# Kernel tuning notes

Hardware: AMD Instinct MI355X
Metric: run time of the kernel (lower is better)

## Reference

```python
import jax, jax.numpy as jnp
import numpy as np

LAMBDA_SOFTMAX = 10.0  # opt.lambda_softmax
LEAKY_SLOPE = 0.1


def l2norm(x, axis):
    # matches torch F.normalize(p=2, eps=1e-12)
    n = jnp.linalg.norm(x, axis=axis, keepdims=True)
    return x / jnp.clip(n, 1e-12)


def setup_inputs() -> dict:
    key = jax.random.key(0)
    k1, k2, k3, k4, k5 = jax.random.split(key, 5)
    I, Q, T, S, D = 64, 49, 64, 64, 256  # n_img, n_region, n_txt, max_words, feature_size
    return {
        "local_img_query": jax.random.normal(k1, (I, Q, D), jnp.float32),
        "local_img_value": jax.random.normal(k2, (I, Q, D), jnp.float32),
        "local_text_key": jax.random.normal(k3, (T, S, D), jnp.float32),
        "local_text_value": jax.random.normal(k4, (T, S, D), jnp.float32),
        "text_length": jax.random.randint(k5, (T,), 8, S + 1, jnp.int32),
    }


def reference(local_img_query, local_img_value, local_text_key, local_text_value, text_length):
    # Vectorized form of the per-sentence Python loop in compute_i2t_sim.
    # Variable sentence lengths are handled with a mask over the padded word axis,
    # which reproduces the ragged torch math exactly (see comments).
    T, S, D = local_text_key.shape
    I, Q, _ = local_img_query.shape

    qn = l2norm(local_img_query, -1)   # [I,Q,D]
    kn = l2norm(local_text_key, -1)    # [T,S,D]

    # bmm(txt_key_norm, queryT): (B,S,D)x(B,D,Q) -> here [T,I,S,Q]
    attn = jnp.einsum('tsd,iqd->tisq', kn, qn)
    attn = jnp.where(attn > 0, attn, LEAKY_SLOPE * attn)      # LeakyReLU(0.1)
    # l2norm(attn, 2) normalizes over queryL per (t,i,s) row -> independent of padding
    attn = l2norm(attn, -1)
    attn = jnp.swapaxes(attn, 2, 3)                            # [T,I,Q,S]

    mask = jnp.arange(S)[None, :] < text_length[:, None]       # [T,S]
    logits = jnp.where(mask[:, None, None, :], attn * LAMBDA_SOFTMAX, -jnp.inf)
    attn = jax.nn.softmax(logits, axis=-1)                     # padded words -> exactly 0

    # focal_equal with sourceL = actual n_word of each sentence
    n_word = text_length.astype(attn.dtype)[:, None, None, None]
    funcF = attn * n_word - jnp.sum(attn, axis=-1, keepdims=True)
    fattn = (funcF > 0).astype(attn.dtype)                     # padded attn=0 -> funcF<0 -> 0
    tmp = fattn * attn
    attn = tmp / jnp.sum(tmp, axis=-1, keepdims=True)

    # bmm(valueT, attnT) -> weighted text context per (txt, img): [T,I,Q,D]
    wei = jnp.einsum('tsd,tiqs->tiqd', local_text_value, attn)
    wei = l2norm(wei, -1)

    # cosine similarity with image values along d, then mean over regions
    v = local_img_value[None]                                  # [1,I,Q,D]
    w12 = jnp.sum(v * wei, -1)
    denom = jnp.linalg.norm(v, axis=-1) * jnp.linalg.norm(wei, axis=-1)
    sim = w12 / jnp.clip(denom, 1e-8)                          # [T,I,Q]
    i2t = sim.mean(axis=-1)                                    # [T,I]
    return i2t.T                                               # [n_img, n_txt]
```

## Files before the change

### kernel.cpp

```cpp
#include <hip/hip_runtime.h>
#include <math.h>

#define I_N 64
#define Q_N 49
#define T_N 64
#define S_N 64
#define D_N 256

typedef __attribute__((ext_vector_type(8))) short short8;
typedef __attribute__((ext_vector_type(4))) float f32x4;
typedef unsigned short ushort_t;

__device__ __forceinline__ float waveReduceSum64(float v) {
    v += __shfl_xor(v, 1);
    v += __shfl_xor(v, 2);
    v += __shfl_xor(v, 4);
    v += __shfl_xor(v, 8);
    v += __shfl_xor(v, 16);
    v += __shfl_xor(v, 32);
    return v;
}

__device__ __forceinline__ ushort_t f2bf(float x) {
    unsigned u = __builtin_bit_cast(unsigned, x);
    unsigned r = (u + 0x7fffu + ((u >> 16) & 1u)) >> 16;
    return (ushort_t)r;
}
__device__ __forceinline__ float bf2f(ushort_t h) {
    unsigned u = ((unsigned)h) << 16;
    return __builtin_bit_cast(float, u);
}
__device__ __forceinline__ void split_bf16(float x, ushort_t& h, ushort_t& l) {
    h = f2bf(x);
    l = f2bf(x - bf2f(h));
}

__global__ void prep_norm(const float* __restrict__ q_in, const float* __restrict__ v_in,
                          const float* __restrict__ k_in,
                          ushort_t* __restrict__ qfh, ushort_t* __restrict__ qfl,
                          ushort_t* __restrict__ kfh, ushort_t* __restrict__ kfl,
                          float* __restrict__ vnorm) {
    int b = blockIdx.x;
    int tid = threadIdx.x;
    int isimg = (b < 4096) ? 1 : 0;
    int row = isimg ? b : (b - 4096);
    int hi = row >> 6, lo = row & 63;
    float x = 0.0f, vv = 0.0f;
    if (isimg) {
        if (lo < Q_N) {
            size_t base = ((size_t)hi * Q_N + lo) * D_N + tid;
            x = q_in[base];
            vv = v_in[base];
        }
    } else {
        x = k_in[(size_t)row * D_N + tid];
    }
    __shared__ float ws[8];
    float s1 = waveReduceSum64(x * x);
    float s2 = waveReduceSum64(vv * vv);
    int wv = tid >> 6, ln = tid & 63;
    if (ln == 0) { ws[wv] = s1; ws[4 + wv] = s2; }
    __syncthreads();
    float n1 = sqrtf(ws[0] + ws[1] + ws[2] + ws[3]);
    float xn = x / fmaxf(n1, 1e-12f);
    ushort_t h, l;
    split_bf16(xn, h, l);
    size_t off = ((size_t)hi << 14) + (size_t)((((lo >> 4) * 8 + (tid >> 5))) << 9)
               + (size_t)(((((tid >> 3) & 3) * 16 + (lo & 15))) << 3) + (tid & 7);
    if (isimg) {
        qfh[off] = h;
        qfl[off] = l;
        if (tid == 0) vnorm[row] = sqrtf(ws[4] + ws[5] + ws[6] + ws[7]);
    } else {
        kfh[off] = h;
        kfl[off] = l;
    }
}

__global__ void prep_vt(const float* __restrict__ tv,
                        ushort_t* __restrict__ vfh, ushort_t* __restrict__ vfl) {
    __shared__ float tile[64][65];
    int t = blockIdx.x;
    int d0 = blockIdx.y * 64;
    int tid = threadIdx.x;
    const float* src = tv + ((size_t)t << 14) + d0;
    ushort_t* dh = vfh + ((size_t)t << 14);
    ushort_t* dl = vfl + ((size_t)t << 14);
#pragma unroll
    for (int r = 0; r < 16; ++r) {
        int idx = r * 256 + tid;
        int s = idx >> 6, d = idx & 63;
        tile[s][d] = src[s * D_N + d];
    }
    __syncthreads();
#pragma unroll
    for (int r = 0; r < 16; ++r) {
        int idx = r * 256 + tid;
        int d = idx >> 6, s = idx & 63;
        int dg = d0 + d;
        float x = tile[s][d];
        ushort_t h, l;
        split_bf16(x, h, l);
        int w = dg >> 5, md = (dg >> 4) & 1, lrd = dg & 15;
        int k0g = s >> 5, lk = (s >> 3) & 3, e = s & 7;
        size_t off = (size_t)(w << 11) + (k0g << 10) + (md << 9) + lk * 128 + lrd * 8 + e;
        dh[off] = h;
        dl[off] = l;
    }
}

__global__ void prep_vp(const float* __restrict__ vimg, float* __restrict__ vP) {
    int i = blockIdx.x;
    int tid = threadIdx.x;
    const float* src = vimg + (size_t)i * Q_N * D_N;
    float* dst = vP + ((size_t)i << 14);
#pragma unroll
    for (int rep = 0; rep < 2; ++rep) {
        int p = rep * 256 + tid;
        int w = p >> 6, lane = p & 63;
        int lr = lane & 15, lk = lane >> 4;
        float* d0 = dst + (size_t)p * 32;
#pragma unroll
        for (int nq = 0; nq < 4; ++nq) {
            int q = nq * 16 + lr;
#pragma unroll
            for (int md = 0; md < 2; ++md)
#pragma unroll
                for (int r = 0; r < 4; ++r) {
                    int d = w * 32 + md * 16 + lk * 4 + r;
                    d0[nq * 8 + md * 4 + r] = (q < Q_N) ? src[q * D_N + d] : 0.0f;
                }
        }
    }
}

__launch_bounds__(512, 6)
__global__ void i2t_mfma(const ushort_t* __restrict__ kfh, const ushort_t* __restrict__ kfl,
                         const ushort_t* __restrict__ qfh, const ushort_t* __restrict__ qfl,
                         const ushort_t* __restrict__ vfh, const ushort_t* __restrict__ vfl,
                         const float* __restrict__ vP,
                         const float* __restrict__ vnorm,
                         const int* __restrict__ tlen,
                         float* __restrict__ out)
{
    __shared__ __align__(16) unsigned char RK[33280];

    const int bid = blockIdx.x;
    const int xcd = bid & 7;
    const int j = bid >> 3;
    const int t = (xcd << 3) | (j & 7);
    const int i = j >> 3;

    const int tid = threadIdx.x;
    const int lane = tid & 63;
    const int w = tid >> 6;
    const int lr = lane & 15;
    const int lk = lane >> 4;

    const int wsr = (w >> 2) * 32;
    const int wq  = (w & 3) * 16;
    f32x4 acc[2];
    acc[0] = (f32x4){0.f, 0.f, 0.f, 0.f};
    acc[1] = (f32x4){0.f, 0.f, 0.f, 0.f};
    {
        const ushort_t* kH = kfh + ((size_t)t << 14) + (size_t)(w >> 2) * 8192;
        const ushort_t* kL = kfl + ((size_t)t << 14) + (size_t)(w >> 2) * 8192;
        const ushort_t* qH = qfh + ((size_t)i << 14) + (size_t)(w & 3) * 4096;
        const ushort_t* qL = qfl + ((size_t)i << 14) + (size_t)(w & 3) * 4096;
#pragma unroll
        for (int k8 = 0; k8 < 8; ++k8) {
            int fo = k8 * 512 + lane * 8;
            short8 aH0 = *(const short8*)(kH + fo);
            short8 aL0 = *(const short8*)(kL + fo);
            short8 aH1 = *(const short8*)(kH + 4096 + fo);
            short8 aL1 = *(const short8*)(kL + 4096 + fo);
            short8 bH  = *(const short8*)(qH + fo);
            short8 bL  = *(const short8*)(qL + fo);
            acc[0] = __builtin_amdgcn_mfma_f32_16x16x32_bf16(aH0, bH, acc[0], 0, 0, 0);
            acc[0] = __builtin_amdgcn_mfma_f32_16x16x32_bf16(aH0, bL, acc[0], 0, 0, 0);
            acc[0] = __builtin_amdgcn_mfma_f32_16x16x32_bf16(aL0, bH, acc[0], 0, 0, 0);
            acc[1] = __builtin_amdgcn_mfma_f32_16x16x32_bf16(aH1, bH, acc[1], 0, 0, 0);
            acc[1] = __builtin_amdgcn_mfma_f32_16x16x32_bf16(aH1, bL, acc[1], 0, 0, 0);
            acc[1] = __builtin_amdgcn_mfma_f32_16x16x32_bf16(aL1, bH, acc[1], 0, 0, 0);
        }
    }
    {
        float* As = (float*)RK;
#pragma unroll
        for (int mi = 0; mi < 2; ++mi)
#pragma unroll
            for (int r = 0; r < 4; ++r) {
                int s = wsr + mi * 16 + lk * 4 + r;
                int q = wq + lr;
                float v = acc[mi][r];
                v = (v > 0.0f) ? v : 0.1f * v;
                As[s * 65 + q] = v;
            }
    }
    __syncthreads();

    {
        const float* As = (const float*)RK;
        float* rinv = (float*)(RK + 16640);
        int s = tid >> 3, part = tid & 7;
        float ss = 0.0f;
#pragma unroll
        for (int q0 = 0; q0 < 64; q0 += 8) {
            float v = As[s * 65 + q0 + part];
            ss += v * v;
        }
        ss += __shfl_xor(ss, 1);
        ss += __shfl_xor(ss, 2);
        ss += __shfl_xor(ss, 4);
        if (part == 0) rinv[s] = 1.0f / fmaxf(sqrtf(ss), 1e-12f);
    }
    __syncthreads();

    const int len = tlen[t];
    {
        const float* As = (const float*)RK;
        const float* rinv = (const float*)(RK + 16640);
        ushort_t* Ph = (ushort_t*)(RK + 16896);
        ushort_t* Pl = (ushort_t*)(RK + 25088);
        const float thr = 1.0f / (float)len;
        int q = tid >> 3, part = tid & 7;
        float logit[8];
        float m = -INFINITY;
#pragma unroll
        for (int k = 0; k < 8; ++k) {
            int s = part * 8 + k;
            float lg = (s < len) ? 10.0f * As[s * 65 + q] * rinv[s] : -INFINITY;
            logit[k] = lg;
            m = fmaxf(m, lg);
        }
        m = fmaxf(m, __shfl_xor(m, 1));
        m = fmaxf(m, __shfl_xor(m, 2));
        m = fmaxf(m, __shfl_xor(m, 4));
        float p[8];
        float sum = 0.0f;
#pragma unroll
        for (int k = 0; k < 8; ++k) {
            int s = part * 8 + k;
            float e = (s < len) ? __expf(logit[k] - m) : 0.0f;
            p[k] = e;
            sum += e;
        }
        sum += __shfl_xor(sum, 1);
        sum += __shfl_xor(sum, 2);
        sum += __shfl_xor(sum, 4);
        float inv = 1.0f / sum;
        float sk = 0.0f;
#pragma unroll
        for (int k = 0; k < 8; ++k) {
            p[k] *= inv;
            if (p[k] > thr) sk += p[k];
        }
        sk += __shfl_xor(sk, 1);
        sk += __shfl_xor(sk, 2);
        sk += __shfl_xor(sk, 4);
        float iv2 = 1.0f / sk;

        short8 vh, vl;
#pragma unroll
        for (int k = 0; k < 8; ++k) {
            float pv = (p[k] > thr) ? p[k] * iv2 : 0.0f;
            if (q >= Q_N) pv = 0.0f;
            ushort_t hh, ll;
            split_bf16(pv, hh, ll);
            vh[k] = (short)hh;
            vl[k] = (short)ll;
        }
        int o = q * 64 + ((part ^ (q & 7)) << 3);
        *(short8*)(Ph + o) = vh;
        *(short8*)(Pl + o) = vl;
    }
    __syncthreads();

    f32x4 acc2[4][2];
#pragma unroll
    for (int a = 0; a < 4; ++a)
#pragma unroll
        for (int b = 0; b < 2; ++b) acc2[a][b] = (f32x4){0.f, 0.f, 0.f, 0.f};
    {
        const ushort_t* vH = vfh + ((size_t)t << 14) + (size_t)w * 2048;
        const ushort_t* vL = vfl + ((size_t)t << 14) + (size_t)w * 2048;
        const ushort_t* PH = (const ushort_t*)(RK + 16896);
        const ushort_t* PL = (const ushort_t*)(RK + 25088);
#pragma unroll
        for (int k0g = 0; k0g < 2; ++k0g) {
#pragma unroll
            for (int md = 0; md < 2; ++md) {
                int vo = k0g * 1024 + md * 512 + lane * 8;
                short8 vh = *(const short8*)(vH + vo);
                short8 vl = *(const short8*)(vL + vo);
#pragma unroll
                for (int nq = 0; nq < 4; ++nq) {
                    int q = nq * 16 + lr;
                    int o = q * 64 + (((k0g * 4 + lk) ^ (q & 7)) << 3);
                    short8 ph = *(const short8*)(PH + o);
                    short8 pl = *(const short8*)(PL + o);
                    acc2[nq][md] = __builtin_amdgcn_mfma_f32_16x16x32_bf16(vh, ph, acc2[nq][md], 0, 0, 0);
                    acc2[nq][md] = __builtin_amdgcn_mfma_f32_16x16x32_bf16(vl, ph, acc2[nq][md], 0, 0, 0);
                    acc2[nq][md] = __builtin_amdgcn_mfma_f32_16x16x32_bf16(vh, pl, acc2[nq][md], 0, 0, 0);
                }
            }
        }
    }

    {
        float* wsq = (float*)RK;
        float* wdv = (float*)(RK + 2048);
        const float* vPb = vP + ((((size_t)i * 8 + w) * 64 + lane) << 5);
#pragma unroll
        for (int nq = 0; nq < 4; ++nq) {
            f32x4 v0 = *(const f32x4*)(vPb + nq * 8);
            f32x4 v1 = *(const f32x4*)(vPb + nq * 8 + 4);
            float s2 = 0.0f, dv = 0.0f;
#pragma unroll
            for (int r = 0; r < 4; ++r) {
                float w0 = acc2[nq][0][r];
                float w1 = acc2[nq][1][r];
                s2 += w0 * w0 + w1 * w1;
                dv += w0 * v0[r] + w1 * v1[r];
            }
            s2 += __shfl_xor(s2, 16);
            s2 += __shfl_xor(s2, 32);
            dv += __shfl_xor(dv, 16);
            dv += __shfl_xor(dv, 32);
            if (lane < 16) {
                wsq[w * 64 + nq * 16 + lane] = s2;
                wdv[w * 64 + nq * 16 + lane] = dv;
            }
        }
    }
    __syncthreads();
    if (tid < 64) {
        const float* wsq = (const float*)RK;
        const float* wdv = (const float*)(RK + 2048);
        int q = tid;
        float s2 = 0.0f, dv = 0.0f;
#pragma unroll
        for (int ww = 0; ww < 8; ++ww) {
            s2 += wsq[ww * 64 + q];
            dv += wdv[ww * 64 + q];
        }
        float sim = 0.0f;
        if (q < Q_N) {
            float wn = sqrtf(s2);
            float w12 = dv / fmaxf(wn, 1e-12f);
            float wnn = wn / fmaxf(wn, 1e-12f);
            float denom = fmaxf(vnorm[i * 64 + q] * wnn, 1e-8f);
            sim = w12 / denom;
        }
        sim = waveReduceSum64(sim);
        if (tid == 0) out[(size_t)i * T_N + t] = sim * (1.0f / (float)Q_N);
    }
}

extern "C" void kernel_launch(void* const* d_in, const int* in_sizes, int n_in,
                              void* d_out, int out_size, void* d_ws, size_t ws_size,
                              hipStream_t stream) {
    const float* img_query = (const float*)d_in[0];
    const float* img_value = (const float*)d_in[1];
    const float* text_key  = (const float*)d_in[2];
    const float* text_val  = (const float*)d_in[3];
    const int*   text_len  = (const int*)d_in[4];
    float* out = (float*)d_out;

    const size_t NPAD = (size_t)64 * 64 * 256;
    ushort_t* qfh = (ushort_t*)d_ws;
    ushort_t* qfl = qfh + NPAD;
    ushort_t* kfh = qfl + NPAD;
    ushort_t* kfl = kfh + NPAD;
    ushort_t* vfh = kfl + NPAD;
    ushort_t* vfl = vfh + NPAD;
    float* vnorm  = (float*)(vfl + NPAD);
    float* vP     = vnorm + I_N * 64;

    prep_norm<<<8192, 256, 0, stream>>>(img_query, img_value, text_key,
                                        qfh, qfl, kfh, kfl, vnorm);
    prep_vt<<<dim3(T_N, 4), 256, 0, stream>>>(text_val, vfh, vfl);
    prep_vp<<<I_N, 256, 0, stream>>>(img_value, vP);

    i2t_mfma<<<T_N * I_N, 512, 0, stream>>>(kfh, kfl, qfh, qfl, vfh, vfl,
                                            vP, vnorm, text_len, out);
}
```

Before: 129.1 us.

## Halve block size to 4 waves with larger per-wave MFMA tiles and fragment reuse

The main kernel now runs 256 threads (4 waves) per block instead of 512. Each wave computes a 32x32 output tile in the first GEMM and covers 64 feature columns in the second, so loaded A/B fragments and softmax P fragments are reused across more MFMAs. The prep kernels change the V-text and V-image packed layouts to match the new per-wave ownership, and the softmax stage uses 4 threads per row instead of 8. In exchange each wave holds more registers (acc2 grows to 16 f32x4) and occupancy per CU may drop.

```diff
diff --git a/kernel.cpp b/kernel.cpp
--- a/kernel.cpp
+++ b/kernel.cpp
@@ -101,9 +101,9 @@
         float x = tile[s][d];
         ushort_t h, l;
         split_bf16(x, h, l);
-        int w = dg >> 5, md = (dg >> 4) & 1, lrd = dg & 15;
-        int k0g = s >> 5, lk = (s >> 3) & 3, e = s & 7;
-        size_t off = (size_t)(w << 11) + (k0g << 10) + (md << 9) + lk * 128 + lrd * 8 + e;
+        int dgrp = dg >> 4, lrd = dg & 15;
+        int k0g = s >> 5, lk3 = (s >> 3) & 3, e = s & 7;
+        size_t off = (size_t)(dgrp << 10) + (k0g << 9) + ((lk3 * 16 + lrd) << 3) + e;
         dh[off] = h;
         dl[off] = l;
     }
@@ -113,28 +113,23 @@
     int i = blockIdx.x;
     int tid = threadIdx.x;
     const float* src = vimg + (size_t)i * Q_N * D_N;
-    float* dst = vP + ((size_t)i << 14);
-#pragma unroll
-    for (int rep = 0; rep < 2; ++rep) {
-        int p = rep * 256 + tid;
-        int w = p >> 6, lane = p & 63;
-        int lr = lane & 15, lk = lane >> 4;
-        float* d0 = dst + (size_t)p * 32;
-#pragma unroll
-        for (int nq = 0; nq < 4; ++nq) {
-            int q = nq * 16 + lr;
-#pragma unroll
-            for (int md = 0; md < 2; ++md)
-#pragma unroll
-                for (int r = 0; r < 4; ++r) {
-                    int d = w * 32 + md * 16 + lk * 4 + r;
-                    d0[nq * 8 + md * 4 + r] = (q < Q_N) ? src[q * D_N + d] : 0.0f;
-                }
-        }
-    }
-}
-
-__launch_bounds__(512, 6)
+    int wv = tid >> 6, lane = tid & 63;
+    int lr = lane & 15, lk = lane >> 4;
+    float* d0 = vP + ((size_t)i << 14) + (size_t)tid * 64;
+#pragma unroll
+    for (int nq = 0; nq < 4; ++nq) {
+        int q = nq * 16 + lr;
+#pragma unroll
+        for (int md = 0; md < 4; ++md)
+#pragma unroll
+            for (int r = 0; r < 4; ++r) {
+                int d = wv * 64 + md * 16 + lk * 4 + r;
+                d0[nq * 16 + md * 4 + r] = (q < Q_N) ? src[q * D_N + d] : 0.0f;
+            }
+    }
+}
+
+__launch_bounds__(256, 4)
 __global__ void i2t_mfma(const ushort_t* __restrict__ kfh, const ushort_t* __restrict__ kfl,
                          const ushort_t* __restrict__ qfh, const ushort_t* __restrict__ qfl,
                          const ushort_t* __restrict__ vfh, const ushort_t* __restrict__ vfl,
@@ -157,16 +152,18 @@
     const int lr = lane & 15;
     const int lk = lane >> 4;
 
-    const int wsr = (w >> 2) * 32;
-    const int wq  = (w & 3) * 16;
-    f32x4 acc[2];
-    acc[0] = (f32x4){0.f, 0.f, 0.f, 0.f};
-    acc[1] = (f32x4){0.f, 0.f, 0.f, 0.f};
-    {
-        const ushort_t* kH = kfh + ((size_t)t << 14) + (size_t)(w >> 2) * 8192;
-        const ushort_t* kL = kfl + ((size_t)t << 14) + (size_t)(w >> 2) * 8192;
-        const ushort_t* qH = qfh + ((size_t)i << 14) + (size_t)(w & 3) * 4096;
-        const ushort_t* qL = qfl + ((size_t)i << 14) + (size_t)(w & 3) * 4096;
+    const int wsr = (w >> 1) * 32;
+    const int wq  = (w & 1) * 32;
+    f32x4 acc[2][2];
+#pragma unroll
+    for (int a = 0; a < 2; ++a)
+#pragma unroll
+        for (int b = 0; b < 2; ++b) acc[a][b] = (f32x4){0.f, 0.f, 0.f, 0.f};
+    {
+        const ushort_t* kH = kfh + ((size_t)t << 14) + (size_t)(w >> 1) * 8192;
+        const ushort_t* kL = kfl + ((size_t)t << 14) + (size_t)(w >> 1) * 8192;
+        const ushort_t* qH = qfh + ((size_t)i << 14) + (size_t)(w & 1) * 8192;
+        const ushort_t* qL = qfl + ((size_t)i << 14) + (size_t)(w & 1) * 8192;
 #pragma unroll
         for (int k8 = 0; k8 < 8; ++k8) {
             int fo = k8 * 512 + lane * 8;
@@ -174,44 +171,53 @@
             short8 aL0 = *(const short8*)(kL + fo);
             short8 aH1 = *(const short8*)(kH + 4096 + fo);
             short8 aL1 = *(const short8*)(kL + 4096 + fo);
-            short8 bH  = *(const short8*)(qH + fo);
-            short8 bL  = *(const short8*)(qL + fo);
-            acc[0] = __builtin_amdgcn_mfma_f32_16x16x32_bf16(aH0, bH, acc[0], 0, 0, 0);
-            acc[0] = __builtin_amdgcn_mfma_f32_16x16x32_bf16(aH0, bL, acc[0], 0, 0, 0);
-            acc[0] = __builtin_amdgcn_mfma_f32_16x16x32_bf16(aL0, bH, acc[0], 0, 0, 0);
-            acc[1] = __builtin_amdgcn_mfma_f32_16x16x32_bf16(aH1, bH, acc[1], 0, 0, 0);
-            acc[1] = __builtin_amdgcn_mfma_f32_16x16x32_bf16(aH1, bL, acc[1], 0, 0, 0);
-            acc[1] = __builtin_amdgcn_mfma_f32_16x16x32_bf16(aL1, bH, acc[1], 0, 0, 0);
+            short8 bH0 = *(const short8*)(qH + fo);
+            short8 bL0 = *(const short8*)(qL + fo);
+            short8 bH1 = *(const short8*)(qH + 4096 + fo);
+            short8 bL1 = *(const short8*)(qL + 4096 + fo);
+            acc[0][0] = __builtin_amdgcn_mfma_f32_16x16x32_bf16(aH0, bH0, acc[0][0], 0, 0, 0);
+            acc[0][1] = __builtin_amdgcn_mfma_f32_16x16x32_bf16(aH0, bH1, acc[0][1], 0, 0, 0);
+            acc[1][0] = __builtin_amdgcn_mfma_f32_16x16x32_bf16(aH1, bH0, acc[1][0], 0, 0, 0);
+            acc[1][1] = __builtin_amdgcn_mfma_f32_16x16x32_bf16(aH1, bH1, acc[1][1], 0, 0, 0);
+            acc[0][0] = __builtin_amdgcn_mfma_f32_16x16x32_bf16(aH0, bL0, acc[0][0], 0, 0, 0);
+            acc[0][1] = __builtin_amdgcn_mfma_f32_16x16x32_bf16(aH0, bL1, acc[0][1], 0, 0, 0);
+            acc[1][0] = __builtin_amdgcn_mfma_f32_16x16x32_bf16(aH1, bL0, acc[1][0], 0, 0, 0);
+            acc[1][1] = __builtin_amdgcn_mfma_f32_16x16x32_bf16(aH1, bL1, acc[1][1], 0, 0, 0);
+            acc[0][0] = __builtin_amdgcn_mfma_f32_16x16x32_bf16(aL0, bH0, acc[0][0], 0, 0, 0);
+            acc[0][1] = __builtin_amdgcn_mfma_f32_16x16x32_bf16(aL0, bH1, acc[0][1], 0, 0, 0);
+            acc[1][0] = __builtin_amdgcn_mfma_f32_16x16x32_bf16(aL1, bH0, acc[1][0], 0, 0, 0);
+            acc[1][1] = __builtin_amdgcn_mfma_f32_16x16x32_bf16(aL1, bH1, acc[1][1], 0, 0, 0);
         }
     }
     {
         float* As = (float*)RK;
 #pragma unroll
-        for (int mi = 0; mi < 2; ++mi)
-#pragma unroll
-            for (int r = 0; r < 4; ++r) {
-                int s = wsr + mi * 16 + lk * 4 + r;
-                int q = wq + lr;
-                float v = acc[mi][r];
-                v = (v > 0.0f) ? v : 0.1f * v;
-                As[s * 65 + q] = v;
-            }
+        for (int si = 0; si < 2; ++si)
+#pragma unroll
+            for (int qi = 0; qi < 2; ++qi)
+#pragma unroll
+                for (int r = 0; r < 4; ++r) {
+                    int s = wsr + si * 16 + lk * 4 + r;
+                    int q = wq + qi * 16 + lr;
+                    float v = acc[si][qi][r];
+                    v = (v > 0.0f) ? v : 0.1f * v;
+                    As[s * 65 + q] = v;
+                }
     }
     __syncthreads();
 
     {
         const float* As = (const float*)RK;
         float* rinv = (float*)(RK + 16640);
-        int s = tid >> 3, part = tid & 7;
+        int s = tid >> 2, part = tid & 3;
         float ss = 0.0f;
 #pragma unroll
-        for (int q0 = 0; q0 < 64; q0 += 8) {
+        for (int q0 = 0; q0 < 64; q0 += 4) {
             float v = As[s * 65 + q0 + part];
             ss += v * v;
         }
         ss += __shfl_xor(ss, 1);
         ss += __shfl_xor(ss, 2);
-        ss += __shfl_xor(ss, 4);
         if (part == 0) rinv[s] = 1.0f / fmaxf(sqrtf(ss), 1e-12f);
     }
     __syncthreads();
@@ -223,85 +229,91 @@
         ushort_t* Ph = (ushort_t*)(RK + 16896);
         ushort_t* Pl = (ushort_t*)(RK + 25088);
         const float thr = 1.0f / (float)len;
-        int q = tid >> 3, part = tid & 7;
-        float logit[8];
+        int q = tid >> 2, part = tid & 3;
+        float logit[16];
         float m = -INFINITY;
 #pragma unroll
-        for (int k = 0; k < 8; ++k) {
-            int s = part * 8 + k;
+        for (int k = 0; k < 16; ++k) {
+            int s = part * 16 + k;
             float lg = (s < len) ? 10.0f * As[s * 65 + q] * rinv[s] : -INFINITY;
             logit[k] = lg;
             m = fmaxf(m, lg);
         }
         m = fmaxf(m, __shfl_xor(m, 1));
         m = fmaxf(m, __shfl_xor(m, 2));
-        m = fmaxf(m, __shfl_xor(m, 4));
-        float p[8];
+        float p[16];
         float sum = 0.0f;
 #pragma unroll
-        for (int k = 0; k < 8; ++k) {
-            int s = part * 8 + k;
+        for (int k = 0; k < 16; ++k) {
+            int s = part * 16 + k;
             float e = (s < len) ? __expf(logit[k] - m) : 0.0f;
             p[k] = e;
             sum += e;
         }
         sum += __shfl_xor(sum, 1);
         sum += __shfl_xor(sum, 2);
-        sum += __shfl_xor(sum, 4);
         float inv = 1.0f / sum;
         float sk = 0.0f;
 #pragma unroll
-        for (int k = 0; k < 8; ++k) {
+        for (int k = 0; k < 16; ++k) {
             p[k] *= inv;
             if (p[k] > thr) sk += p[k];
         }
         sk += __shfl_xor(sk, 1);
         sk += __shfl_xor(sk, 2);
-        sk += __shfl_xor(sk, 4);
         float iv2 = 1.0f / sk;
 
-        short8 vh, vl;
-#pragma unroll
-        for (int k = 0; k < 8; ++k) {
+        ushort_t hh[16], ll[16];
+#pragma unroll
+        for (int k = 0; k < 16; ++k) {
             float pv = (p[k] > thr) ? p[k] * iv2 : 0.0f;
             if (q >= Q_N) pv = 0.0f;
-            ushort_t hh, ll;
-            split_bf16(pv, hh, ll);
-            vh[k] = (short)hh;
-            vl[k] = (short)ll;
-        }
-        int o = q * 64 + ((part ^ (q & 7)) << 3);
-        *(short8*)(Ph + o) = vh;
-        *(short8*)(Pl + o) = vl;
-    }
-    __syncthreads();
-
-    f32x4 acc2[4][2];
+            split_bf16(pv, hh[k], ll[k]);
+        }
+        int c0 = (2 * part) ^ (q & 7);
+        int c1 = (2 * part + 1) ^ (q & 7);
+        short8 v0, v1;
+#pragma unroll
+        for (int k = 0; k < 8; ++k) { v0[k] = (short)hh[k]; v1[k] = (short)hh[k + 8]; }
+        *(short8*)(Ph + q * 64 + (c0 << 3)) = v0;
+        *(short8*)(Ph + q * 64 + (c1 << 3)) = v1;
+#pragma unroll
+        for (int k = 0; k < 8; ++k) { v0[k] = (short)ll[k]; v1[k] = (short)ll[k + 8]; }
+        *(short8*)(Pl + q * 64 + (c0 << 3)) = v0;
+        *(short8*)(Pl + q * 64 + (c1 << 3)) = v1;
+    }
+    __syncthreads();
+
+    f32x4 acc2[4][4];
 #pragma unroll
     for (int a = 0; a < 4; ++a)
 #pragma unroll
-        for (int b = 0; b < 2; ++b) acc2[a][b] = (f32x4){0.f, 0.f, 0.f, 0.f};
-    {
-        const ushort_t* vH = vfh + ((size_t)t << 14) + (size_t)w * 2048;
-        const ushort_t* vL = vfl + ((size_t)t << 14) + (size_t)w * 2048;
+        for (int b = 0; b < 4; ++b) acc2[a][b] = (f32x4){0.f, 0.f, 0.f, 0.f};
+    {
+        const ushort_t* vH = vfh + ((size_t)t << 14) + (size_t)w * 4096;
+        const ushort_t* vL = vfl + ((size_t)t << 14) + (size_t)w * 4096;
         const ushort_t* PH = (const ushort_t*)(RK + 16896);
         const ushort_t* PL = (const ushort_t*)(RK + 25088);
 #pragma unroll
         for (int k0g = 0; k0g < 2; ++k0g) {
-#pragma unroll
-            for (int md = 0; md < 2; ++md) {
-                int vo = k0g * 1024 + md * 512 + lane * 8;
+            short8 ph[4], pl[4];
+#pragma unroll
+            for (int nq = 0; nq < 4; ++nq) {
+                int qrow = nq * 16 + lr;
+                int o = qrow * 64 + (((k0g * 4 + lk) ^ (qrow & 7)) << 3);
+                ph[nq] = *(const short8*)(PH + o);
+                pl[nq] = *(const short8*)(PL + o);
+            }
+#pragma unroll
+            for (int md = 0; md < 4; ++md) {
+                int vo = md * 1024 + k0g * 512 + lane * 8;
                 short8 vh = *(const short8*)(vH + vo);
                 short8 vl = *(const short8*)(vL + vo);
 #pragma unroll
                 for (int nq = 0; nq < 4; ++nq) {
-                    int q = nq * 16 + lr;
-                    int o = q * 64 + (((k0g * 4 + lk) ^ (q & 7)) << 3);
-                    short8 ph = *(const short8*)(PH + o);
-                    short8 pl = *(const short8*)(PL + o);
-                    acc2[nq][md] = __builtin_amdgcn_mfma_f32_16x16x32_bf16(vh, ph, acc2[nq][md], 0, 0, 0);
-                    acc2[nq][md] = __builtin_amdgcn_mfma_f32_16x16x32_bf16(vl, ph, acc2[nq][md], 0, 0, 0);
-                    acc2[nq][md] = __builtin_amdgcn_mfma_f32_16x16x32_bf16(vh, pl, acc2[nq][md], 0, 0, 0);
+                    acc2[md][nq] = __builtin_amdgcn_mfma_f32_16x16x32_bf16(vh, ph[nq], acc2[md][nq], 0, 0, 0);
+                    acc2[md][nq] = __builtin_amdgcn_mfma_f32_16x16x32_bf16(vl, ph[nq], acc2[md][nq], 0, 0, 0);
+                    acc2[md][nq] = __builtin_amdgcn_mfma_f32_16x16x32_bf16(vh, pl[nq], acc2[md][nq], 0, 0, 0);
                 }
             }
         }
@@ -309,19 +321,20 @@
 
     {
         float* wsq = (float*)RK;
-        float* wdv = (float*)(RK + 2048);
-        const float* vPb = vP + ((((size_t)i * 8 + w) * 64 + lane) << 5);
+        float* wdv = (float*)(RK + 1024);
+        const float* vPb = vP + ((((size_t)i * 4 + w) * 64 + lane) << 6);
 #pragma unroll
         for (int nq = 0; nq < 4; ++nq) {
-            f32x4 v0 = *(const f32x4*)(vPb + nq * 8);
-            f32x4 v1 = *(const f32x4*)(vPb + nq * 8 + 4);
             float s2 = 0.0f, dv = 0.0f;
 #pragma unroll
-            for (int r = 0; r < 4; ++r) {
-                float w0 = acc2[nq][0][r];
-                float w1 = acc2[nq][1][r];
-                s2 += w0 * w0 + w1 * w1;
-                dv += w0 * v0[r] + w1 * v1[r];
+            for (int md = 0; md < 4; ++md) {
+                f32x4 vv = *(const f32x4*)(vPb + nq * 16 + md * 4);
+#pragma unroll
+                for (int r = 0; r < 4; ++r) {
+                    float wv = acc2[md][nq][r];
+                    s2 += wv * wv;
+                    dv += wv * vv[r];
+                }
             }
             s2 += __shfl_xor(s2, 16);
             s2 += __shfl_xor(s2, 32);
@@ -336,11 +349,11 @@
     __syncthreads();
     if (tid < 64) {
         const float* wsq = (const float*)RK;
-        const float* wdv = (const float*)(RK + 2048);
+        const float* wdv = (const float*)(RK + 1024);
         int q = tid;
         float s2 = 0.0f, dv = 0.0f;
 #pragma unroll
-        for (int ww = 0; ww < 8; ++ww) {
+        for (int ww = 0; ww < 4; ++ww) {
             s2 += wsq[ww * 64 + q];
             dv += wdv[ww * 64 + q];
         }
@@ -382,6 +395,6 @@
     prep_vt<<<dim3(T_N, 4), 256, 0, stream>>>(text_val, vfh, vfl);
     prep_vp<<<I_N, 256, 0, stream>>>(img_value, vP);
 
-    i2t_mfma<<<T_N * I_N, 512, 0, stream>>>(kfh, kfl, qfh, qfl, vfh, vfl,
+    i2t_mfma<<<T_N * I_N, 256, 0, stream>>>(kfh, kfl, qfh, qfl, vfh, vfl,
                                             vP, vnorm, text_len, out);
 }
```

Result: faster. 112.3 us (-13.0%).
